# Performance work log

Hardware: AMD Instinct MI355X
Metric: run time of the kernel (lower is better)

The kernel has to match this reference:

```python
import jax, jax.numpy as jnp
import numpy as np
from jax import lax

VOCAB = 35095 + 2
WORD_DIM = 300
MAX_SENT = 3000
N_FILT = 100
N_CLASSES = 10


def setup_inputs() -> dict:
    key = jax.random.key(0)
    ks = jax.random.split(key, 10)
    x = jax.random.randint(ks[0], (2, MAX_SENT), 0, VOCAB)
    emb = jax.random.normal(ks[1], (VOCAB, WORD_DIM), dtype=jnp.float32) * 0.1
    emb = emb.at[0].set(0.0)  # padding_idx=0
    w1 = jax.random.normal(ks[2], (N_FILT, 1, 3), dtype=jnp.float32) * 0.1
    b1 = jax.random.normal(ks[3], (N_FILT,), dtype=jnp.float32) * 0.01
    w2 = jax.random.normal(ks[4], (N_FILT, 1, 4), dtype=jnp.float32) * 0.1
    b2 = jax.random.normal(ks[5], (N_FILT,), dtype=jnp.float32) * 0.01
    w3 = jax.random.normal(ks[6], (N_FILT, 1, 5), dtype=jnp.float32) * 0.1
    b3 = jax.random.normal(ks[7], (N_FILT,), dtype=jnp.float32) * 0.01
    fc_w = jax.random.normal(ks[8], (N_CLASSES, 3 * N_FILT), dtype=jnp.float32) * 0.05
    fc_b = jax.random.normal(ks[9], (N_CLASSES,), dtype=jnp.float32) * 0.01
    return {"x": x, "emb": emb, "w1": w1, "b1": b1, "w2": w2, "b2": b2,
            "w3": w3, "b3": b3, "fc_w": fc_w, "fc_b": fc_b}


def _conv_relu_maxpool(h, w, b):
    # h: [B, 1, L]; w: [F, 1, K]  ->  [B, F]
    y = lax.conv_general_dilated(h, w, window_strides=(1,), padding='VALID',
                                 dimension_numbers=('NCW', 'OIW', 'NCW'))
    y = jnp.maximum(y + b[None, :, None], 0.0)
    return jnp.max(y, axis=2)


def reference(x, emb, w1, b1, w2, b2, w3, b3, fc_w, fc_b):
    # Embedding lookup then flatten to a single-channel 1D signal of length 900k
    h = emb[x].reshape(-1, 1, WORD_DIM * MAX_SENT)  # [B, 1, 900000]
    c1 = _conv_relu_maxpool(h, w1, b1)  # [B, 100]
    c2 = _conv_relu_maxpool(h, w2, b2)
    c3 = _conv_relu_maxpool(h, w3, b3)
    feats = jnp.concatenate([c1, c2, c3], axis=1)  # [B, 300]
    # Dropout is identity at inference
    return feats @ fc_w.T + fc_b
```

## Files before the change

### kernel.cpp

```cpp
#include <hip/hip_runtime.h>

#define VOCAB   35097
#define DDIM    300
#define NWORDS  3000
#define L_SIG   900000
#define NFILT   100
#define NCLS    10

#define QQ      28
#define HALF    14
#define WIN     (QQ + 4)
#define NHP     (HALF + 4)
#define BLK_POS (64 * QQ)
#define NBLKA   503
#define NBLKP   512
#define FPG     5
#define NGRPW   5

typedef __attribute__((ext_vector_type(2))) float f32x2;

__device__ __forceinline__ float relu_(float v) { return fmaxf(v, 0.0f); }

__device__ __forceinline__ f32x2 pk_mul(f32x2 a, f32x2 b) {
  f32x2 d;
  asm("v_pk_mul_f32 %0, %1, %2" : "=v"(d) : "v"(a), "v"(b));
  return d;
}
__device__ __forceinline__ f32x2 pk_fma(f32x2 a, f32x2 b, f32x2 c) {
  f32x2 d;
  asm("v_pk_fma_f32 %0, %1, %2, %3" : "=v"(d) : "v"(a), "v"(b), "v"(c));
  return d;
}
__device__ __forceinline__ f32x2 dup2(float w) { f32x2 d; d.x = w; d.y = w; return d; }

template<bool TAIL>
__device__ __forceinline__ void run_group(
    const float (&h)[WIN], const f32x2 (&hp)[NHP], int t0, int f0, int lane,
    const float* __restrict__ w1, const float* __restrict__ w2,
    const float* __restrict__ w3,
    float* __restrict__ pslot)
{
  int n3 = QQ, n4 = QQ, n5 = QQ;
  if (TAIL) {
    n3 = min(max(899998 - t0, 0), QQ);
    n4 = min(max(899997 - t0, 0), QQ);
    n5 = min(max(899996 - t0, 0), QQ);
  }
  const float NEG = -__builtin_huge_valf();

  float a3[FPG], a4[FPG], a5[FPG];

  #pragma unroll
  for (int j = 0; j < FPG; ++j) {
    const int fu = __builtin_amdgcn_readfirstlane(f0 + j);
    const float a0 = w1[fu*3+0], a1 = w1[fu*3+1], a2 = w1[fu*3+2];
    const float c0 = w2[fu*4+0], c1 = w2[fu*4+1], c2 = w2[fu*4+2], c3 = w2[fu*4+3];
    const float e0 = w3[fu*5+0], e1 = w3[fu*5+1], e2 = w3[fu*5+2], e3 = w3[fu*5+3], e4 = w3[fu*5+4];

    float m3a = NEG, m3b = NEG, m4a = NEG, m4b = NEG, m5a = NEG, m5b = NEG;

    if (!TAIL) {
      const f32x2 pa0 = dup2(a0), pa1 = dup2(a1), pa2 = dup2(a2);
      const f32x2 pc0 = dup2(c0), pc1 = dup2(c1), pc2 = dup2(c2), pc3 = dup2(c3);
      const f32x2 pe0 = dup2(e0), pe1 = dup2(e1), pe2 = dup2(e2), pe3 = dup2(e3), pe4 = dup2(e4);

      #pragma unroll
      for (int p = 0; p < HALF; ++p) {
        f32x2 t3 = pk_mul(pa2, hp[p+2]);
        t3 = pk_fma(pa1, hp[p+1], t3);
        t3 = pk_fma(pa0, hp[p+0], t3);
        f32x2 t4 = pk_mul(pc3, hp[p+3]);
        t4 = pk_fma(pc2, hp[p+2], t4);
        t4 = pk_fma(pc1, hp[p+1], t4);
        t4 = pk_fma(pc0, hp[p+0], t4);
        f32x2 t5 = pk_mul(pe4, hp[p+4]);
        t5 = pk_fma(pe3, hp[p+3], t5);
        t5 = pk_fma(pe2, hp[p+2], t5);
        t5 = pk_fma(pe1, hp[p+1], t5);
        t5 = pk_fma(pe0, hp[p+0], t5);
        if (p & 1) {
          m3b = fmaxf(fmaxf(m3b, t3.x), t3.y);
          m4b = fmaxf(fmaxf(m4b, t4.x), t4.y);
          m5b = fmaxf(fmaxf(m5b, t5.x), t5.y);
        } else {
          m3a = fmaxf(fmaxf(m3a, t3.x), t3.y);
          m4a = fmaxf(fmaxf(m4a, t4.x), t4.y);
          m5a = fmaxf(fmaxf(m5a, t5.x), t5.y);
        }
      }
    } else {
      #pragma unroll
      for (int p = 0; p < QQ; ++p) {
        float v3 = fmaf(a0, h[p], fmaf(a1, h[p+1], a2 * h[p+2]));
        float v4 = fmaf(c0, h[p], fmaf(c1, h[p+1], fmaf(c2, h[p+2], c3 * h[p+3])));
        float v5 = fmaf(e0, h[p], fmaf(e1, h[p+1], fmaf(e2, h[p+2], fmaf(e3, h[p+3], e4 * h[p+4]))));
        if (p < n3) { if (p & 1) m3b = fmaxf(m3b, v3); else m3a = fmaxf(m3a, v3); }
        if (p < n4) { if (p & 1) m4b = fmaxf(m4b, v4); else m4a = fmaxf(m4a, v4); }
        if (p < n5) { if (p & 1) m5b = fmaxf(m5b, v5); else m5a = fmaxf(m5a, v5); }
      }
    }
    a3[j] = fmaxf(m3a, m3b);
    a4[j] = fmaxf(m4a, m4b);
    a5[j] = fmaxf(m5a, m5b);
  }

  #pragma unroll
  for (int s = 1; s < 64; s <<= 1) {
    #pragma unroll
    for (int j = 0; j < FPG; ++j) {
      a3[j] = fmaxf(a3[j], __shfl_xor(a3[j], s));
      a4[j] = fmaxf(a4[j], __shfl_xor(a4[j], s));
      a5[j] = fmaxf(a5[j], __shfl_xor(a5[j], s));
    }
  }

  if (lane == 0) {
    #pragma unroll
    for (int j = 0; j < FPG; ++j) {
      pslot[(size_t)(j)      * NBLKP] = a3[j];
      pslot[(size_t)(5 + j)  * NBLKP] = a4[j];
      pslot[(size_t)(10 + j) * NBLKP] = a5[j];
    }
  }
}

__global__ __launch_bounds__(256, 4) void conv_max_kernel(
    const int* __restrict__ x, const float* __restrict__ emb,
    const float* __restrict__ w1, const float* __restrict__ w2,
    const float* __restrict__ w3,
    float* __restrict__ partial)
{
  const int lane  = threadIdx.x & 63;
  const int wave  = threadIdx.x >> 6;
  const int batch = blockIdx.y;
  const int t0_blk = blockIdx.x * BLK_POS;
  const int t0     = t0_blk + lane * QQ;
  const int fbase  = wave * (FPG * NGRPW);

  float h[WIN];
  {
    int w0 = t0 / DDIM;
    int d0 = t0 - w0 * DDIM;
    int wa = min(w0, NWORDS - 1);
    int wb = min(w0 + 1, NWORDS - 1);
    int xa = x[batch * NWORDS + wa];
    int xb = x[batch * NWORDS + wb];
    const float4* rowA = (const float4*)(emb + (size_t)xa * DDIM) + (d0 >> 2);
    const float4* rowB = (const float4*)(emb + (size_t)xb * DDIM);
    const int nf4 = (DDIM - d0) >> 2;
    #pragma unroll
    for (int i = 0; i < WIN / 4; ++i) {
      const float4* src = (i < nf4) ? (rowA + i) : (rowB + (i - nf4));
      float4 v = *src;
      h[4*i+0] = v.x; h[4*i+1] = v.y; h[4*i+2] = v.z; h[4*i+3] = v.w;
    }
  }

  f32x2 hp[NHP];
  #pragma unroll
  for (int k = 0; k < NHP; ++k) { f32x2 t; t.x = h[k]; t.y = h[k + HALF]; hp[k] = t; }

  float* prow = partial + ((size_t)batch * 300 + wave * 75) * NBLKP + blockIdx.x;

  const bool tail = (t0_blk + BLK_POS + 4) > L_SIG;
  if (tail) {
    #pragma unroll 1
    for (int g = 0; g < NGRPW; ++g)
      run_group<true >(h, hp, t0, fbase + g * FPG, lane, w1, w2, w3,
                       prow + (size_t)g * 15 * NBLKP);
  } else {
    #pragma unroll 1
    for (int g = 0; g < NGRPW; ++g)
      run_group<false>(h, hp, t0, fbase + g * FPG, lane, w1, w2, w3,
                       prow + (size_t)g * 15 * NBLKP);
  }
}

__global__ void reduce_kernel(const float* __restrict__ partial,
                              const float* __restrict__ b1,
                              const float* __restrict__ b2,
                              const float* __restrict__ b3,
                              float* __restrict__ feats)
{
  const int idx  = blockIdx.x;
  const int b    = idx / 300;
  const int p    = idx % 300;
  const int lane = threadIdx.x;

  const int wv = p / 75, r = p % 75, g = r / 15, q = r % 15;
  const int conv = q / 5, j = q % 5;
  const int f = wv * 25 + g * 5 + j;

  const float* row = partial + ((size_t)b * 300 + p) * NBLKP;
  float m = -__builtin_huge_valf();
  for (int i = lane; i < NBLKA; i += 64)
    m = fmaxf(m, row[i]);
  #pragma unroll
  for (int s = 1; s < 64; s <<= 1)
    m = fmaxf(m, __shfl_xor(m, s));

  if (lane == 0) {
    const float bias = (conv == 0) ? b1[f] : (conv == 1) ? b2[f] : b3[f];
    feats[b * 300 + conv * NFILT + f] = relu_(m + bias);
  }
}

__global__ void fc_kernel(const float* __restrict__ feats,
                          const float* __restrict__ fcw,
                          const float* __restrict__ fcb,
                          float* __restrict__ out)
{
  const int b = blockIdx.x / NCLS;
  const int c = blockIdx.x % NCLS;
  const int lane = threadIdx.x;
  float s = 0.0f;
  for (int k = lane; k < 3 * NFILT; k += 64)
    s += feats[b * 3 * NFILT + k] * fcw[c * 3 * NFILT + k];
  #pragma unroll
  for (int k = 1; k < 64; k <<= 1) s += __shfl_xor(s, k);
  if (lane == 0) out[b * NCLS + c] = s + fcb[c];
}

extern "C" void kernel_launch(void* const* d_in, const int* in_sizes, int n_in,
                              void* d_out, int out_size, void* d_ws, size_t ws_size,
                              hipStream_t stream)
{
  const int*   x   = (const int*)  d_in[0];
  const float* emb = (const float*)d_in[1];
  const float* w1  = (const float*)d_in[2];
  const float* b1  = (const float*)d_in[3];
  const float* w2  = (const float*)d_in[4];
  const float* b2  = (const float*)d_in[5];
  const float* w3  = (const float*)d_in[6];
  const float* b3  = (const float*)d_in[7];
  const float* fcw = (const float*)d_in[8];
  const float* fcb = (const float*)d_in[9];
  float* out = (float*)d_out;

  float* partial = (float*)d_ws;
  float* feats   = partial + (size_t)2 * 300 * NBLKP;

  dim3 grid(NBLKA, 2);
  conv_max_kernel<<<grid, 256, 0, stream>>>(x, emb, w1, w2, w3, partial);
  reduce_kernel<<<600, 64, 0, stream>>>(partial, b1, b2, b3, feats);
  fc_kernel<<<2 * NCLS, 64, 0, stream>>>(feats, fcw, fcb, out);
}
```

Measured before the change: 171.2 us.

## Transpose partial-max layout to block-major and reduce per thread column

Partial maxima are now stored block-major, so each block's 300 results sit contiguously instead of being strided by 512 across filter rows. The reduce kernel changes from 600 single-wave blocks doing shuffle reductions to 2 blocks of 320 threads. In those blocks each thread walks one column serially, with loads coalesced across threads and unrolled by 8. This is meant to improve write locality in the conv kernel and to cut reduce launch and shuffle overhead. The trade-off is that only 2 workgroups run the reduction, each thread looping over 503 serial dependent loads, which may leave the GPU badly underused.

```diff
diff --git a/kernel.cpp b/kernel.cpp
--- a/kernel.cpp
+++ b/kernel.cpp
@@ -13,7 +13,6 @@
 #define NHP     (HALF + 4)
 #define BLK_POS (64 * QQ)
 #define NBLKA   503
-#define NBLKP   512
 #define FPG     5
 #define NGRPW   5
 
@@ -117,9 +116,9 @@
   if (lane == 0) {
     #pragma unroll
     for (int j = 0; j < FPG; ++j) {
-      pslot[(size_t)(j)      * NBLKP] = a3[j];
-      pslot[(size_t)(5 + j)  * NBLKP] = a4[j];
-      pslot[(size_t)(10 + j) * NBLKP] = a5[j];
+      pslot[j]      = a3[j];
+      pslot[5 + j]  = a4[j];
+      pslot[10 + j] = a5[j];
     }
   }
 }
@@ -160,49 +159,56 @@
   #pragma unroll
   for (int k = 0; k < NHP; ++k) { f32x2 t; t.x = h[k]; t.y = h[k + HALF]; hp[k] = t; }
 
-  float* prow = partial + ((size_t)batch * 300 + wave * 75) * NBLKP + blockIdx.x;
+  float* pwave = partial + ((size_t)batch * NBLKA + blockIdx.x) * 300 + wave * 75;
 
   const bool tail = (t0_blk + BLK_POS + 4) > L_SIG;
   if (tail) {
     #pragma unroll 1
     for (int g = 0; g < NGRPW; ++g)
-      run_group<true >(h, hp, t0, fbase + g * FPG, lane, w1, w2, w3,
-                       prow + (size_t)g * 15 * NBLKP);
+      run_group<true >(h, hp, t0, fbase + g * FPG, lane, w1, w2, w3, pwave + g * 15);
   } else {
     #pragma unroll 1
     for (int g = 0; g < NGRPW; ++g)
-      run_group<false>(h, hp, t0, fbase + g * FPG, lane, w1, w2, w3,
-                       prow + (size_t)g * 15 * NBLKP);
-  }
-}
-
-__global__ void reduce_kernel(const float* __restrict__ partial,
-                              const float* __restrict__ b1,
-                              const float* __restrict__ b2,
-                              const float* __restrict__ b3,
-                              float* __restrict__ feats)
-{
-  const int idx  = blockIdx.x;
-  const int b    = idx / 300;
-  const int p    = idx % 300;
-  const int lane = threadIdx.x;
+      run_group<false>(h, hp, t0, fbase + g * FPG, lane, w1, w2, w3, pwave + g * 15);
+  }
+}
+
+__global__ __launch_bounds__(320) void reduce_kernel(
+    const float* __restrict__ partial,
+    const float* __restrict__ b1,
+    const float* __restrict__ b2,
+    const float* __restrict__ b3,
+    float* __restrict__ feats)
+{
+  const int b = blockIdx.x;
+  const int p = threadIdx.x;
+  if (p >= 300) return;
+
+  const float* col = partial + (size_t)b * NBLKA * 300 + p;
+  float m = -__builtin_huge_valf();
+  int i = 0;
+  for (; i + 8 <= NBLKA; i += 8) {
+    float v0 = col[(size_t)(i+0) * 300];
+    float v1 = col[(size_t)(i+1) * 300];
+    float v2 = col[(size_t)(i+2) * 300];
+    float v3 = col[(size_t)(i+3) * 300];
+    float v4 = col[(size_t)(i+4) * 300];
+    float v5 = col[(size_t)(i+5) * 300];
+    float v6 = col[(size_t)(i+6) * 300];
+    float v7 = col[(size_t)(i+7) * 300];
+    m = fmaxf(fmaxf(m, v0), v1);
+    m = fmaxf(fmaxf(m, v2), v3);
+    m = fmaxf(fmaxf(m, v4), v5);
+    m = fmaxf(fmaxf(m, v6), v7);
+  }
+  for (; i < NBLKA; ++i)
+    m = fmaxf(m, col[(size_t)i * 300]);
 
   const int wv = p / 75, r = p % 75, g = r / 15, q = r % 15;
   const int conv = q / 5, j = q % 5;
   const int f = wv * 25 + g * 5 + j;
-
-  const float* row = partial + ((size_t)b * 300 + p) * NBLKP;
-  float m = -__builtin_huge_valf();
-  for (int i = lane; i < NBLKA; i += 64)
-    m = fmaxf(m, row[i]);
-  #pragma unroll
-  for (int s = 1; s < 64; s <<= 1)
-    m = fmaxf(m, __shfl_xor(m, s));
-
-  if (lane == 0) {
-    const float bias = (conv == 0) ? b1[f] : (conv == 1) ? b2[f] : b3[f];
-    feats[b * 300 + conv * NFILT + f] = relu_(m + bias);
-  }
+  const float bias = (conv == 0) ? b1[f] : (conv == 1) ? b2[f] : b3[f];
+  feats[b * 300 + conv * NFILT + f] = relu_(m + bias);
 }
 
 __global__ void fc_kernel(const float* __restrict__ feats,
@@ -238,10 +244,10 @@
   float* out = (float*)d_out;
 
   float* partial = (float*)d_ws;
-  float* feats   = partial + (size_t)2 * 300 * NBLKP;
+  float* feats   = partial + (size_t)2 * NBLKA * 300;
 
   dim3 grid(NBLKA, 2);
   conv_max_kernel<<<grid, 256, 0, stream>>>(x, emb, w1, w2, w3, partial);
-  reduce_kernel<<<600, 64, 0, stream>>>(partial, b1, b2, b3, feats);
+  reduce_kernel<<<2, 320, 0, stream>>>(partial, b1, b2, b3, feats);
   fc_kernel<<<2 * NCLS, 64, 0, stream>>>(feats, fcw, fcb, out);
 }
```

After: 183.7 us. 1.07x slower.
